# Kernel tuning notes

Measured on AMD Instinct MI355X. Metric: run time of the kernel, lower is better.

The kernel has to match this reference:

```python
import jax, jax.numpy as jnp
import numpy as np

N = 6144
IN_DIM = 256
OUT_DIM = 256
NUM_HEADS = 4
HEAD_DIM = OUT_DIM // NUM_HEADS  # 64
NEG_SLOPE = 0.2


def setup_inputs() -> dict:
    key = jax.random.key(0)
    k_x, k_adj, k_W, k_a = jax.random.split(key, 4)
    x = jax.random.normal(k_x, (N, IN_DIM), dtype=jnp.float32)
    adj = jax.random.randint(k_adj, (N, N), 0, 2, dtype=jnp.int32)
    # nn.Linear(in_dim, out_dim, bias=False): store as [in_dim, out_dim] so y = x @ W
    W = jax.random.normal(k_W, (IN_DIM, OUT_DIM), dtype=jnp.float32) / np.sqrt(IN_DIM)
    # nn.Linear(2*head_dim, 1, bias=False): a single attention vector shared across heads
    a = jax.random.normal(k_a, (2 * HEAD_DIM,), dtype=jnp.float32) / np.sqrt(2 * HEAD_DIM)
    return {"x": x, "adj": adj, "W": W, "a": a}


def reference(x, adj, W, a):
    n = x.shape[0]
    Wh = (x @ W).reshape(n, NUM_HEADS, HEAD_DIM)  # (N, H, D)
    a_src, a_dst = a[:HEAD_DIM], a[HEAD_DIM:]
    # score[h,i,j] = leaky_relu(a_src . Wh[i,h] + a_dst . Wh[j,h])
    f_src = jnp.einsum('nhd,d->hn', Wh, a_src)  # (H, N)
    f_dst = jnp.einsum('nhd,d->hn', Wh, a_dst)  # (H, N)
    e = f_src[:, :, None] + f_dst[:, None, :]   # (H, N, N)
    e = jnp.where(e > 0, e, NEG_SLOPE * e)      # LeakyReLU(0.2)
    mask = (adj != 0)[None, :, :]               # (1, N, N)
    e = jnp.where(mask, e, -jnp.inf)
    alpha = jax.nn.softmax(e, axis=-1)          # (H, N, N)
    alpha = jnp.nan_to_num(alpha, nan=0.0)      # empty rows -> 0 (matches torch)
    # dropout: eval mode (identity)
    out = jnp.einsum('hij,jhd->ihd', alpha, Wh).reshape(n, OUT_DIM)
    return out
```

## Files before the change

kernel.cpp:

```cpp
#include <hip/hip_runtime.h>

#define NN 6144
#define SHIFTC (12.0f*1.4426950408889634f)
#define LOG2E 1.4426950408889634f

typedef float f32x4 __attribute__((ext_vector_type(4)));
typedef short short8 __attribute__((ext_vector_type(8)));
typedef int   i32x4 __attribute__((ext_vector_type(4)));

__device__ __forceinline__ float bf2f(unsigned short u){
  return __uint_as_float(((unsigned int)u)<<16);
}
__device__ __forceinline__ unsigned short f2bf(float f){
  unsigned int x = __float_as_uint(f);
  x += 0x7fffu + ((x>>16)&1u);
  return (unsigned short)(x>>16);
}

__global__ __launch_bounds__(256) void k_gemm(const float* __restrict__ x,
                                              const float* __restrict__ W,
                                              unsigned short* __restrict__ wht){
  __shared__ float sx[16*256];
  const int t = threadIdx.x;
  const int i0 = blockIdx.x * 16;
  {
    const int r = t >> 4, kc = t & 15;
    const float* src = x + (size_t)(i0 + r)*256 + kc*16;
    float* dst = sx + r*256 + kc*16;
#pragma unroll
    for (int q = 0; q < 4; ++q)
      *reinterpret_cast<f32x4*>(dst + 4*q) = *reinterpret_cast<const f32x4*>(src + 4*q);
  }
  __syncthreads();
  float acc[16];
#pragma unroll
  for (int r = 0; r < 16; ++r) acc[r] = 0.f;
  for (int k = 0; k < 256; k += 4) {
    const float w0 = W[(size_t)(k+0)*256 + t];
    const float w1 = W[(size_t)(k+1)*256 + t];
    const float w2 = W[(size_t)(k+2)*256 + t];
    const float w3 = W[(size_t)(k+3)*256 + t];
#pragma unroll
    for (int r = 0; r < 16; ++r) {
      f32x4 xv = *reinterpret_cast<const f32x4*>(sx + r*256 + k);
      acc[r] = fmaf(xv.x, w0, acc[r]);
      acc[r] = fmaf(xv.y, w1, acc[r]);
      acc[r] = fmaf(xv.z, w2, acc[r]);
      acc[r] = fmaf(xv.w, w3, acc[r]);
    }
  }
  alignas(16) unsigned short buf[16];
#pragma unroll
  for (int r = 0; r < 16; ++r) buf[r] = f2bf(acc[r]);
  unsigned short* dst = wht + (size_t)t*NN + i0;
  *reinterpret_cast<uint4*>(dst)     = *reinterpret_cast<const uint4*>(buf);
  *reinterpret_cast<uint4*>(dst + 8) = *reinterpret_cast<const uint4*>(buf + 8);
}

__global__ __launch_bounds__(256) void k_f(const unsigned short* __restrict__ wht,
                                           const float* __restrict__ a,
                                           float* __restrict__ fs2,
                                           float* __restrict__ edp,
                                           float* __restrict__ edn){
  __shared__ unsigned short sw[256*64];
  const int t = threadIdx.x;
  const int i0 = blockIdx.x * 64;
  {
    const unsigned short* src = wht + (size_t)t*NN + i0;
    unsigned short* dst = sw + t*64;
#pragma unroll
    for (int q = 0; q < 8; ++q)
      *reinterpret_cast<uint4*>(dst + q*8) = *reinterpret_cast<const uint4*>(src + q*8);
  }
  __syncthreads();
  const int ii = t & 63, h = t >> 6;
  float s_ = 0.f, d_ = 0.f;
#pragma unroll 16
  for (int d = 0; d < 64; ++d) {
    const float v = bf2f(sw[(h*64 + d)*64 + ii]);
    s_ = fmaf(v, a[d],      s_);
    d_ = fmaf(v, a[64 + d], d_);
  }
  const float fs2v = s_ * LOG2E;
  const float fd2v = d_ * LOG2E;
  fs2[(size_t)h*NN + i0 + ii] = fs2v;
  edp[(size_t)h*NN + i0 + ii] = exp2f(fd2v - SHIFTC);
  edn[(size_t)h*NN + i0 + ii] = exp2f(0.2f * fd2v);
}

__global__ __launch_bounds__(256) void k_attn(const int* __restrict__ adj,
                                              const unsigned short* __restrict__ wht,
                                              const float* __restrict__ fs2,
                                              const float* __restrict__ edp,
                                              const float* __restrict__ edn,
                                              float* __restrict__ apart,
                                              float* __restrict__ lpart,
                                              int nsteps){
  __shared__ unsigned short swht[2][64*72];
  __shared__ unsigned int   smask[2][128];
  __shared__ float          sedp[2][64];
  __shared__ float          sedn[2][64];
  const int t  = threadIdx.x;
  const int w  = t >> 6, l = t & 63, lr = l & 15, hi = l >> 4;
  const int bid = blockIdx.x;
  const int h   = (bid >> 3) & 3;
  const int g   = (bid & 7) | ((bid >> 5) << 3);
  const int it  = g % 96;
  const int js  = g / 96;
  const int i0 = it * 64;
  const int jbase = js * nsteps * 64;
  const int i_row = i0 + w*16 + lr;

  const float fsv  = fs2[(size_t)h*NN + i_row];
  const float EiNh = exp2f(-0.8f*fsv - SHIFTC);

  f32x4 acc[4];
#pragma unroll
  for (int q = 0; q < 4; ++q) acc[q] = (f32x4){0.f,0.f,0.f,0.f};
  float ls = 0.f;

  const int r_ = t >> 2, ch_ = t & 3;
  const int* asrc = adj + (size_t)(i0 + r_)*NN + jbase + ch_*16;
  const unsigned short* wsrc = wht + (size_t)(h*64 + r_)*NN + jbase + ch_*16;
  const float* pesrc = edp + (size_t)h*NN + jbase;
  const float* nesrc = edn + (size_t)h*NN + jbase;

  {
    i32x4 aj[4];
#pragma unroll
    for (int q = 0; q < 4; ++q) aj[q] = *reinterpret_cast<const i32x4*>(asrc + q*4);
    const uint4 wv0 = *reinterpret_cast<const uint4*>(wsrc);
    const uint4 wv1 = *reinterpret_cast<const uint4*>(wsrc + 8);
    unsigned int bits = 0u;
#pragma unroll
    for (int q = 0; q < 4; ++q) {
      bits |= ((unsigned)aj[q].x) << (q*4 + 0);
      bits |= ((unsigned)aj[q].y) << (q*4 + 1);
      bits |= ((unsigned)aj[q].z) << (q*4 + 2);
      bits |= ((unsigned)aj[q].w) << (q*4 + 3);
    }
    unsigned short* dst = &swht[0][r_*72 + ch_*16];
    *reinterpret_cast<uint4*>(dst)     = wv0;
    *reinterpret_cast<uint4*>(dst + 8) = wv1;
    reinterpret_cast<unsigned short*>(smask[0])[r_*4 + ch_] = (unsigned short)bits;
    if (t < 64) { sedp[0][t] = pesrc[t]; }
    else if (t < 128) { sedn[0][t - 64] = nesrc[t - 64]; }
  }
  __syncthreads();

  for (int st = 0; st < nsteps; ++st) {
    const int cur = st & 1, nxt = cur ^ 1;
    const bool pf = (st + 1) < nsteps;

    i32x4 ajp[4]; uint4 wvp0, wvp1; float pep = 0.f, nep = 0.f;
    if (pf) {
      const int o = (st + 1) * 64;
#pragma unroll
      for (int q = 0; q < 4; ++q)
        ajp[q] = *reinterpret_cast<const i32x4*>(asrc + o + q*4);
      wvp0 = *reinterpret_cast<const uint4*>(wsrc + o);
      wvp1 = *reinterpret_cast<const uint4*>(wsrc + o + 8);
      if (t < 64) { pep = pesrc[o + t]; }
      else if (t < 128) { nep = nesrc[o + t - 64]; }
    }

    const unsigned int m0 = smask[cur][(w*16 + lr)*2 + 0];
    const unsigned int m1 = smask[cur][(w*16 + lr)*2 + 1];
    float maskf[16];
#pragma unroll
    for (int e = 0; e < 8; ++e) {
      maskf[e]     = (float)((m0 >> (8*hi + e)) & 1u);
      maskf[8 + e] = (float)((m1 >> (8*hi + e)) & 1u);
    }
    const f32x4 ep0 = *reinterpret_cast<const f32x4*>(&sedp[cur][8*hi + 0]);
    const f32x4 ep1 = *reinterpret_cast<const f32x4*>(&sedp[cur][8*hi + 4]);
    const f32x4 ep2 = *reinterpret_cast<const f32x4*>(&sedp[cur][32 + 8*hi + 0]);
    const f32x4 ep3 = *reinterpret_cast<const f32x4*>(&sedp[cur][32 + 8*hi + 4]);
    const f32x4 en0 = *reinterpret_cast<const f32x4*>(&sedn[cur][8*hi + 0]);
    const f32x4 en1 = *reinterpret_cast<const f32x4*>(&sedn[cur][8*hi + 4]);
    const f32x4 en2 = *reinterpret_cast<const f32x4*>(&sedn[cur][32 + 8*hi + 0]);
    const f32x4 en3 = *reinterpret_cast<const f32x4*>(&sedn[cur][32 + 8*hi + 4]);
    float p[16];
#pragma unroll
    for (int e = 0; e < 4; ++e) {
      p[e]      = maskf[e]      * fmaxf(ep0[e], EiNh * en0[e]);
      p[4 + e]  = maskf[4 + e]  * fmaxf(ep1[e], EiNh * en1[e]);
      p[8 + e]  = maskf[8 + e]  * fmaxf(ep2[e], EiNh * en2[e]);
      p[12 + e] = maskf[12 + e] * fmaxf(ep3[e], EiNh * en3[e]);
    }
    float lsh = 0.f;
#pragma unroll
    for (int e = 0; e < 16; ++e) lsh += p[e];
    ls += lsh;
    int4 aw0, aw1;
    asm("v_cvt_pk_bf16_f32 %0, %1, %2" : "=v"(aw0.x) : "v"(p[0]),  "v"(p[1]));
    asm("v_cvt_pk_bf16_f32 %0, %1, %2" : "=v"(aw0.y) : "v"(p[2]),  "v"(p[3]));
    asm("v_cvt_pk_bf16_f32 %0, %1, %2" : "=v"(aw0.z) : "v"(p[4]),  "v"(p[5]));
    asm("v_cvt_pk_bf16_f32 %0, %1, %2" : "=v"(aw0.w) : "v"(p[6]),  "v"(p[7]));
    asm("v_cvt_pk_bf16_f32 %0, %1, %2" : "=v"(aw1.x) : "v"(p[8]),  "v"(p[9]));
    asm("v_cvt_pk_bf16_f32 %0, %1, %2" : "=v"(aw1.y) : "v"(p[10]), "v"(p[11]));
    asm("v_cvt_pk_bf16_f32 %0, %1, %2" : "=v"(aw1.z) : "v"(p[12]), "v"(p[13]));
    asm("v_cvt_pk_bf16_f32 %0, %1, %2" : "=v"(aw1.w) : "v"(p[14]), "v"(p[15]));
    const short8 af0 = __builtin_bit_cast(short8, aw0);
    const short8 af1 = __builtin_bit_cast(short8, aw1);
#pragma unroll
    for (int nc = 0; nc < 4; ++nc) {
      const unsigned short* bp = &swht[cur][(nc*16 + lr)*72 + 8*hi];
      const short8 b0 = *reinterpret_cast<const short8*>(bp);
      const short8 b1 = *reinterpret_cast<const short8*>(bp + 32);
      acc[nc] = __builtin_amdgcn_mfma_f32_16x16x32_bf16(af0, b0, acc[nc], 0, 0, 0);
      acc[nc] = __builtin_amdgcn_mfma_f32_16x16x32_bf16(af1, b1, acc[nc], 0, 0, 0);
    }

    if (pf) {
      unsigned int bits = 0u;
#pragma unroll
      for (int q = 0; q < 4; ++q) {
        bits |= ((unsigned)ajp[q].x) << (q*4 + 0);
        bits |= ((unsigned)ajp[q].y) << (q*4 + 1);
        bits |= ((unsigned)ajp[q].z) << (q*4 + 2);
        bits |= ((unsigned)ajp[q].w) << (q*4 + 3);
      }
      unsigned short* dst = &swht[nxt][r_*72 + ch_*16];
      *reinterpret_cast<uint4*>(dst)     = wvp0;
      *reinterpret_cast<uint4*>(dst + 8) = wvp1;
      reinterpret_cast<unsigned short*>(smask[nxt])[r_*4 + ch_] = (unsigned short)bits;
      if (t < 64) { sedp[nxt][t] = pep; }
      else if (t < 128) { sedn[nxt][t - 64] = nep; }
    }
    __syncthreads();
  }

  {
    float v = ls;
    v += __shfl_xor(v, 16, 64);
    v += __shfl_xor(v, 32, 64);
    ls = v;
  }
  if (hi == 0)
    lpart[((size_t)js*4 + h)*NN + i_row] = ls;
#pragma unroll
  for (int nc = 0; nc < 4; ++nc)
#pragma unroll
    for (int rg = 0; rg < 4; ++rg) {
      const int irow = i0 + w*16 + 4*hi + rg;
      const int col  = h*64 + nc*16 + lr;
      apart[((size_t)js*NN + irow)*256 + col] = acc[nc][rg];
    }
}

__global__ __launch_bounds__(256) void k_comb(const float* __restrict__ apart,
                                              const float* __restrict__ lpart,
                                              float* __restrict__ out,
                                              int jsplit){
  const int idx = blockIdx.x * 256 + threadIdx.x;
  const int i = idx >> 8, c = idx & 255, h = c >> 6;
  float num = 0.f, den = 0.f;
  for (int s = 0; s < jsplit; ++s) {
    num += apart[((size_t)s*NN + i)*256 + c];
    den += lpart[((size_t)s*4 + h)*NN + i];
  }
  out[idx] = (den > 0.f) ? (num / den) : 0.f;
}

extern "C" void kernel_launch(void* const* d_in, const int* in_sizes, int n_in,
                              void* d_out, int out_size, void* d_ws, size_t ws_size,
                              hipStream_t stream) {
  const float* x   = (const float*)d_in[0];
  const int*   adj = (const int*)d_in[1];
  const float* W   = (const float*)d_in[2];
  const float* a   = (const float*)d_in[3];
  float* out = (float*)d_out;
  char* ws = (char*)d_ws;

  size_t off = 0;
  unsigned short* wht = (unsigned short*)(ws + off); off += (size_t)256*NN*2;
  float* fs2 = (float*)(ws + off); off += (size_t)4*NN*4;
  float* edp = (float*)(ws + off); off += (size_t)4*NN*4;
  float* edn = (float*)(ws + off); off += (size_t)4*NN*4;

  int jsplit = 8;
  while (jsplit > 1 &&
         off + (size_t)jsplit*4*NN*4 + (size_t)jsplit*NN*256*4 > ws_size)
    jsplit >>= 1;

  float* lpart = (float*)(ws + off); off += (size_t)jsplit*4*NN*4;
  float* apart = (float*)(ws + off);

  const int nsteps = NN / (jsplit * 64);

  k_gemm<<<dim3(NN/16), dim3(256), 0, stream>>>(x, W, wht);
  k_f   <<<dim3(NN/64), dim3(256), 0, stream>>>(wht, a, fs2, edp, edn);
  k_attn<<<dim3(4*(NN/64)*jsplit), dim3(256), 0, stream>>>(adj, wht, fs2, edp, edn, apart, lpart, nsteps);
  k_comb<<<dim3((out_size + 255)/256), dim3(256), 0, stream>>>(apart, lpart, out, jsplit);
}
```

Measured before the change: 120.1 us.

## Replace split-K partial buffers with atomic accumulation into output

Instead of writing per-split partial numerators and denominators to a large workspace and reducing them in a combine kernel, the attention kernel now atomically adds its partial results directly into the output and a denominator array. A zeroing kernel runs first and a light normalization kernel divides at the end. This removes the write and re-read of about 50MB of partials, at the cost of float atomics (with contention across the 8 splits) and nondeterministic summation order.

Result: slower. 128.4 us (+6.9%).

```diff
diff --git a/kernel.cpp b/kernel.cpp
--- a/kernel.cpp
+++ b/kernel.cpp
@@ -15,6 +15,14 @@
   unsigned int x = __float_as_uint(f);
   x += 0x7fffu + ((x>>16)&1u);
   return (unsigned short)(x>>16);
+}
+
+__global__ __launch_bounds__(256) void k_zero(float* __restrict__ out, int n_out,
+                                              float* __restrict__ den, int n_den){
+  const int idx = blockIdx.x * 256 + threadIdx.x;
+  const int stride = gridDim.x * 256;
+  for (int i = idx; i < n_out; i += stride) out[i] = 0.f;
+  for (int i = idx; i < n_den; i += stride) den[i] = 0.f;
 }
 
 __global__ __launch_bounds__(256) void k_gemm(const float* __restrict__ x,
@@ -93,8 +101,8 @@
                                               const float* __restrict__ fs2,
                                               const float* __restrict__ edp,
                                               const float* __restrict__ edn,
-                                              float* __restrict__ apart,
-                                              float* __restrict__ lpart,
+                                              float* __restrict__ out,
+                                              float* __restrict__ den,
                                               int nsteps){
   __shared__ unsigned short swht[2][64*72];
   __shared__ unsigned int   smask[2][128];
@@ -238,29 +246,24 @@
     ls = v;
   }
   if (hi == 0)
-    lpart[((size_t)js*4 + h)*NN + i_row] = ls;
+    atomicAdd(&den[(size_t)h*NN + i_row], ls);
 #pragma unroll
   for (int nc = 0; nc < 4; ++nc)
 #pragma unroll
     for (int rg = 0; rg < 4; ++rg) {
       const int irow = i0 + w*16 + 4*hi + rg;
       const int col  = h*64 + nc*16 + lr;
-      apart[((size_t)js*NN + irow)*256 + col] = acc[nc][rg];
-    }
-}
-
-__global__ __launch_bounds__(256) void k_comb(const float* __restrict__ apart,
-                                              const float* __restrict__ lpart,
-                                              float* __restrict__ out,
-                                              int jsplit){
+      atomicAdd(&out[(size_t)irow*256 + col], acc[nc][rg]);
+    }
+}
+
+__global__ __launch_bounds__(256) void k_norm(float* __restrict__ out,
+                                              const float* __restrict__ den){
   const int idx = blockIdx.x * 256 + threadIdx.x;
   const int i = idx >> 8, c = idx & 255, h = c >> 6;
-  float num = 0.f, den = 0.f;
-  for (int s = 0; s < jsplit; ++s) {
-    num += apart[((size_t)s*NN + i)*256 + c];
-    den += lpart[((size_t)s*4 + h)*NN + i];
-  }
-  out[idx] = (den > 0.f) ? (num / den) : 0.f;
+  const float d = den[(size_t)h*NN + i];
+  const float v = out[idx];
+  out[idx] = (d > 0.f) ? (v / d) : 0.f;
 }
 
 extern "C" void kernel_launch(void* const* d_in, const int* in_sizes, int n_in,
@@ -278,19 +281,14 @@
   float* fs2 = (float*)(ws + off); off += (size_t)4*NN*4;
   float* edp = (float*)(ws + off); off += (size_t)4*NN*4;
   float* edn = (float*)(ws + off); off += (size_t)4*NN*4;
-
-  int jsplit = 8;
-  while (jsplit > 1 &&
-         off + (size_t)jsplit*4*NN*4 + (size_t)jsplit*NN*256*4 > ws_size)
-    jsplit >>= 1;
-
-  float* lpart = (float*)(ws + off); off += (size_t)jsplit*4*NN*4;
-  float* apart = (float*)(ws + off);
-
+  float* den = (float*)(ws + off); off += (size_t)4*NN*4;
+
+  const int jsplit = 8;
   const int nsteps = NN / (jsplit * 64);
 
+  k_zero<<<dim3(1024), dim3(256), 0, stream>>>(out, out_size, den, 4*NN);
   k_gemm<<<dim3(NN/16), dim3(256), 0, stream>>>(x, W, wht);
   k_f   <<<dim3(NN/64), dim3(256), 0, stream>>>(wht, a, fs2, edp, edn);
-  k_attn<<<dim3(4*(NN/64)*jsplit), dim3(256), 0, stream>>>(adj, wht, fs2, edp, edn, apart, lpart, nsteps);
-  k_comb<<<dim3((out_size + 255)/256), dim3(256), 0, stream>>>(apart, lpart, out, jsplit);
-}
+  k_attn<<<dim3(4*(NN/64)*jsplit), dim3(256), 0, stream>>>(adj, wht, fs2, edp, edn, out, den, nsteps);
+  k_norm<<<dim3((out_size + 255)/256), dim3(256), 0, stream>>>(out, den);
+}
```
